# Kernel optimization log

Hardware: AMD Instinct MI355X
Metric: run time of the kernel (lower is better)

## Reference

```python
import jax, jax.numpy as jnp
import numpy as np
from jax import lax

# pywt db4 decomposition lowpass filter
_DEC_LO_NP = np.array([-0.010597401784997278, 0.032883011666982945,
                        0.030841381835986965, -0.18703481171888114,
                        -0.02798376941698385, 0.6308807679295904,
                        0.7148465705525415, 0.23037781330885523], dtype=np.float32)
_SIGNS = np.array([(-1.0) ** (k + 1) for k in range(8)], dtype=np.float32)
DEC_LO = jnp.asarray(_DEC_LO_NP)                    # dec_lo
DEC_HI = jnp.asarray(_DEC_LO_NP[::-1] * _SIGNS)     # dec_hi (QMF)
LF = 8
MAX_LEVEL = 4
# analysis kernels: torch cross-correlates with reversed dec filters == true conv
H_ANA = jnp.stack([DEC_LO[::-1], DEC_HI[::-1]])[:, None, :]  # (2,1,LF)
# synthesis: torch conv_transpose with rec filters == xcorr(dilated x, flip(rec)) = xcorr with dec
G0F = DEC_LO[None, None, :]
G1F = DEC_HI[None, None, :]
DN = ('NCH', 'OIH', 'NCH')


def _dwt_step(x):
    # x: (N, Lx) -> (lo, hi) each (N, outsize); pytorch_wavelets afb1d, mode='symmetric'
    N = x.shape[-1]
    outsize = (N + LF - 1) // 2          # pywt.dwt_coeff_len
    p = 2 * (outsize - 1) - N + LF
    xp = jnp.pad(x, ((0, 0), (p // 2, (p + 1) // 2)), mode='symmetric')
    y = lax.conv_general_dilated(xp[:, None, :], H_ANA, (2,), 'VALID',
                                 dimension_numbers=DN)  # (N,2,outsize)
    return y[:, 0, :], y[:, 1, :]


def _idwt_step(lo, hi):
    # pytorch_wavelets sfb1d: conv_transpose(stride=2, padding=LF-2)
    # == lhs-dilated xcorr with flipped rec filters (= dec filters), pad 1 each side
    y0 = lax.conv_general_dilated(lo[:, None, :], G0F, (1,), [(1, 1)],
                                  lhs_dilation=(2,), dimension_numbers=DN)
    y1 = lax.conv_general_dilated(hi[:, None, :], G1F, (1,), [(1, 1)],
                                  lhs_dilation=(2,), dimension_numbers=DN)
    return (y0 + y1)[:, 0, :]            # (N, 2*Llo + 2 - LF)


def dywpe(x, proj_w, proj_b, scale_emb, gate_w, gate_b):
    B, L, _ = x.shape
    d_model = scale_emb.shape[1]
    # channel_proj -> mono signal (B, L)
    x_mono = (jnp.einsum('blc,oc->blo', x, proj_w) + proj_b)[..., 0]
    # multi-level DWT
    lo = x_mono
    highs = []
    for _ in range(MAX_LEVEL):
        lo, hi = _dwt_step(lo)
        highs.append(hi)
    # gates: sigmoid(g) * tanh(v), per scale -> (MAX_LEVEL+1, d_model)
    gated = scale_emb @ gate_w.T + gate_b
    g, v = jnp.split(gated, 2, axis=-1)
    gates = jax.nn.sigmoid(g) * jnp.tanh(v)

    def mod(coef, gate):  # (B,Lc) x (d,) -> (B*d, Lc): outer product, fold d into batch
        return (coef[:, None, :] * gate[None, :, None]).reshape(B * d_model, -1)

    x0 = mod(lo, gates[0])
    hs = [mod(highs[i], gates[i + 1]) for i in range(MAX_LEVEL)]
    # IDWT, coarsest level first
    for h in hs[::-1]:
        if x0.shape[-1] > h.shape[-1]:
            x0 = x0[:, :h.shape[-1]]
        x0 = _idwt_step(x0, h)
    pe = x0.reshape(B, d_model, -1).transpose(0, 2, 1)  # (B, L', d_model)
    if pe.shape[1] < L:
        pe = jnp.pad(pe, ((0, 0), (0, L - pe.shape[1]), (0, 0)))
    elif pe.shape[1] > L:
        pe = pe[:, :L]
    return pe


def setup_inputs() -> dict:
    key = jax.random.key(0)
    ks = jax.random.split(key, 6)
    B, L, d_x, d_model, J = 32, 4096, 8, 512, 4
    return {
        'x': jax.random.normal(ks[0], (B, L, d_x), dtype=jnp.float32),
        'proj_w': jax.random.normal(ks[1], (1, d_x), dtype=jnp.float32) * 0.3,
        'proj_b': jax.random.normal(ks[2], (1,), dtype=jnp.float32) * 0.02,
        'scale_emb': jax.random.normal(ks[3], (J + 1, d_model), dtype=jnp.float32),
        'gate_w': jax.random.normal(ks[4], (2 * d_model, d_model), dtype=jnp.float32) * 0.04,
        'gate_b': jax.random.normal(ks[5], (2 * d_model,), dtype=jnp.float32) * 0.02,
    }


def reference(x, proj_w, proj_b, scale_emb, gate_w, gate_b):
    return dywpe(x, proj_w, proj_b, scale_emb, gate_w, gate_b)
```

## Files before the change

kernel.cpp:

```cpp
#include <hip/hip_runtime.h>

#define NB    32
#define LSEQ  4096
#define DM    512
#define ROWS  64
#define CHUNKS (LSEQ / ROWS)

typedef float f32x4 __attribute__((ext_vector_type(4)));

__device__ __constant__ float c_DL[8] = {
    -0.010597401784997278f,  0.032883011666982945f,  0.030841381835986965f,
    -0.18703481171888114f,  -0.02798376941698385f,   0.6308807679295904f,
     0.7148465705525415f,    0.23037781330885523f};
__device__ __constant__ float c_DH[8] = {
    -0.23037781330885523f,   0.7148465705525415f,   -0.6308807679295904f,
    -0.02798376941698385f,   0.18703481171888114f,   0.030841381835986965f,
    -0.032883011666982945f, -0.010597401784997278f};

__device__ __forceinline__ int imin(int a, int b) { return a < b ? a : b; }
__device__ __forceinline__ int imax(int a, int b) { return a > b ? a : b; }

__device__ __forceinline__ int reflect_idx(int i, int N) {
    if (i < 0)  i = -1 - i;
    if (i >= N) i = 2 * N - 1 - i;
    return i;
}

template <bool HI>
__device__ void fwd_range_w(const float* __restrict__ src, int src_lo, int Nsrc,
                            float* __restrict__ dst, int d_lo, int d_hi, int lane) {
    for (int t = d_lo + lane; t <= d_hi; t += 64) {
        int base = 2 * t - 6;
        float acc = 0.f;
#pragma unroll
        for (int k = 0; k < 8; ++k) {
            float xv = src[reflect_idx(base + k, Nsrc) - src_lo];
            acc = fmaf(xv, HI ? c_DH[7 - k] : c_DL[7 - k], acc);
        }
        dst[t - d_lo] = acc;
    }
}

template <bool HI>
__device__ void inv_range_w(const float* __restrict__ c, int c_lo,
                            float* __restrict__ y, int y_lo, int y_hi, int lane) {
    for (int t = y_lo + lane; t <= y_hi; t += 64) {
        int base = (t >> 1) - c_lo;
        int odd = t & 1;
        float f0 = odd ? (HI ? c_DH[0] : c_DL[0]) : (HI ? c_DH[1] : c_DL[1]);
        float f1 = odd ? (HI ? c_DH[2] : c_DL[2]) : (HI ? c_DH[3] : c_DL[3]);
        float f2 = odd ? (HI ? c_DH[4] : c_DL[4]) : (HI ? c_DH[5] : c_DL[5]);
        float f3 = odd ? (HI ? c_DH[6] : c_DL[6]) : (HI ? c_DH[7] : c_DL[7]);
        float acc = c[base] * f0;
        acc = fmaf(c[base + 1], f1, acc);
        acc = fmaf(c[base + 2], f2, acc);
        acc = fmaf(c[base + 3], f3, acc);
        y[t - y_lo] = acc;
    }
}

__global__ __launch_bounds__(1024) void gates_kernel(
    const float* __restrict__ scale_emb, const float* __restrict__ gate_w,
    const float* __restrict__ gate_b, float* __restrict__ gates) {
    int lane = threadIdx.x & 63;
    int c = blockIdx.x * 16 + (threadIdx.x >> 6);
    const float4* rg = (const float4*)(gate_w + (size_t)c * DM) + lane * 2;
    const float4* rv = (const float4*)(gate_w + (size_t)(c + DM) * DM) + lane * 2;
    float4 a0 = rg[0], a1 = rg[1];
    float4 b0 = rv[0], b1 = rv[1];
    float gacc[5], vacc[5];
#pragma unroll
    for (int j = 0; j < 5; ++j) {
        const float4* sj = (const float4*)(scale_emb + (size_t)j * DM) + lane * 2;
        float4 s0 = sj[0], s1 = sj[1];
        float ga;
        ga = s0.x * a0.x;            ga = fmaf(s0.y, a0.y, ga);
        ga = fmaf(s0.z, a0.z, ga);   ga = fmaf(s0.w, a0.w, ga);
        ga = fmaf(s1.x, a1.x, ga);   ga = fmaf(s1.y, a1.y, ga);
        ga = fmaf(s1.z, a1.z, ga);   ga = fmaf(s1.w, a1.w, ga);
        float va;
        va = s0.x * b0.x;            va = fmaf(s0.y, b0.y, va);
        va = fmaf(s0.z, b0.z, va);   va = fmaf(s0.w, b0.w, va);
        va = fmaf(s1.x, b1.x, va);   va = fmaf(s1.y, b1.y, va);
        va = fmaf(s1.z, b1.z, va);   va = fmaf(s1.w, b1.w, va);
        gacc[j] = ga;
        vacc[j] = va;
    }
#pragma unroll
    for (int j = 0; j < 5; ++j) {
#pragma unroll
        for (int off = 32; off > 0; off >>= 1) {
            gacc[j] += __shfl_xor(gacc[j], off, 64);
            vacc[j] += __shfl_xor(vacc[j], off, 64);
        }
    }
    if (lane == 0) {
        float bg = gate_b[c], bv = gate_b[DM + c];
#pragma unroll
        for (int j = 0; j < 5; ++j) {
            float g = gacc[j] + bg;
            float v = vacc[j] + bv;
            float sg = 1.f / (1.f + expf(-g));
            gates[j * DM + c] = sg * tanhf(v);
        }
    }
}

__global__ __launch_bounds__(256, 4) void fused_kernel(
    const float* __restrict__ x, const float* __restrict__ proj_w,
    const float* __restrict__ proj_b, const float* __restrict__ gates,
    float* __restrict__ out) {
    __shared__ float GL[5 * DM];
    __shared__ float XW[288];
    __shared__ float LO1[140], LO2[68], LO3[32];
    __shared__ float HI1[36], H2W[24], H3W[16], L4W[12], H4W[12];
    __shared__ float AW[16], A4W[16], A3W[24], BW[24], B4W[24];
    __shared__ float P0W[36], P2W[36], P3W[36], P4W[36];
    __shared__ float SJ[5 * ROWS];

    int bid = blockIdx.x;
    int b  = bid >> 6;
    int l0 = (bid & 63) * ROWS;

    int p0 = l0 >> 1,  p1 = ((l0 + ROWS - 1) >> 1) + 3;
    int b0 = p0 >> 1,  b1 = (p1 >> 1) + 3;
    int a0 = b0 >> 1,  a1 = (b1 >> 1) + 3;
    int w0 = a0 >> 1,  w1 = (a1 >> 1) + 3;
    int t3lo = imax(imin(imin(2 * w0 - 6, a0), 517), 0);
    int t3hi = imin(imax(imax(2 * w1 + 1, a1), 0), 517);
    int t2lo = imax(imin(2 * t3lo - 6, 2 * a0 - 6), 0);
    int t2hi = imin(imax(2 * t3hi + 1, 2 * a1 + 1), 1028);
    int t1lo = imax(imin(2 * t2lo - 6, 2 * b0 - 6), 0);
    int t1hi = imin(imax(2 * t2hi + 1, 2 * b1 + 1), 2050);
    int txlo = imax(imin(2 * t1lo - 6, 2 * p0 - 6), 0);
    int txhi = imin(imax(2 * t1hi + 1, 2 * p1 + 1), 4095);

    int wid = threadIdx.x >> 6;
    int lane = threadIdx.x & 63;

    if (wid != 0) {
        for (int i = (threadIdx.x - 64); i < 5 * DM / 4; i += 192)
            ((f32x4*)GL)[i] = ((const f32x4*)gates)[i];
    } else {
        float w[8];
#pragma unroll
        for (int k = 0; k < 8; ++k) w[k] = proj_w[k];
        float pb = proj_b[0];
        const float* xb = x + (size_t)b * LSEQ * 8;
        for (int i = txlo + lane; i <= txhi; i += 64) {
            const float4* xv = (const float4*)(xb + (size_t)i * 8);
            float4 q0 = xv[0], q1 = xv[1];
            float acc = pb;
            acc = fmaf(q0.x, w[0], acc); acc = fmaf(q0.y, w[1], acc);
            acc = fmaf(q0.z, w[2], acc); acc = fmaf(q0.w, w[3], acc);
            acc = fmaf(q1.x, w[4], acc); acc = fmaf(q1.y, w[5], acc);
            acc = fmaf(q1.z, w[6], acc); acc = fmaf(q1.w, w[7], acc);
            XW[i - txlo] = acc;
        }
        fwd_range_w<false>(XW, txlo, 4096, LO1, t1lo, t1hi, lane);
        fwd_range_w<true >(XW, txlo, 4096, HI1, p0, p1, lane);
        fwd_range_w<false>(LO1, t1lo, 2051, LO2, t2lo, t2hi, lane);
        fwd_range_w<true >(LO1, t1lo, 2051, H2W, b0, b1, lane);
        fwd_range_w<false>(LO2, t2lo, 1029, LO3, t3lo, t3hi, lane);
        fwd_range_w<true >(LO2, t2lo, 1029, H3W, a0, a1, lane);
        fwd_range_w<false>(LO3, t3lo, 518, L4W, w0, w1, lane);
        fwd_range_w<true >(LO3, t3lo, 518, H4W, w0, w1, lane);
        inv_range_w<false>(L4W, w0, AW,  a0, a1, lane);
        inv_range_w<true >(H4W, w0, A4W, a0, a1, lane);
        inv_range_w<true >(H3W, a0, A3W, b0, b1, lane);
        inv_range_w<true >(H2W, b0, P2W, p0, p1, lane);
        inv_range_w<false>(AW,  a0, BW,  b0, b1, lane);
        inv_range_w<false>(A4W, a0, B4W, b0, b1, lane);
        inv_range_w<false>(A3W, b0, P3W, p0, p1, lane);
        inv_range_w<false>(BW,  b0, P0W, p0, p1, lane);
        inv_range_w<false>(B4W, b0, P4W, p0, p1, lane);
    }
    __syncthreads();

    for (int idx = threadIdx.x; idx < 5 * ROWS; idx += 256) {
        int j = idx >> 6;
        int r = idx & (ROWS - 1);
        int l = l0 + r;
        int base = (l >> 1) - p0;
        int odd = l & 1;
        const float* Pj = (j == 0) ? P0W : (j == 1) ? HI1 :
                          (j == 2) ? P2W : (j == 3) ? P3W : P4W;
        bool hi = (j == 1);
        float f0 = odd ? (hi ? c_DH[0] : c_DL[0]) : (hi ? c_DH[1] : c_DL[1]);
        float f1 = odd ? (hi ? c_DH[2] : c_DL[2]) : (hi ? c_DH[3] : c_DL[3]);
        float f2 = odd ? (hi ? c_DH[4] : c_DL[4]) : (hi ? c_DH[5] : c_DL[5]);
        float f3 = odd ? (hi ? c_DH[6] : c_DL[6]) : (hi ? c_DH[7] : c_DL[7]);
        float acc = Pj[base] * f0;
        acc = fmaf(Pj[base + 1], f1, acc);
        acc = fmaf(Pj[base + 2], f2, acc);
        acc = fmaf(Pj[base + 3], f3, acc);
        SJ[idx] = acc;
    }
    __syncthreads();

    int half = threadIdx.x >> 7;
    int c4 = threadIdx.x & 127;
    f32x4 g0 = ((const f32x4*)(GL + 0 * DM))[c4];
    f32x4 g1 = ((const f32x4*)(GL + 1 * DM))[c4];
    f32x4 g2 = ((const f32x4*)(GL + 2 * DM))[c4];
    f32x4 g3 = ((const f32x4*)(GL + 3 * DM))[c4];
    f32x4 g4 = ((const f32x4*)(GL + 4 * DM))[c4];

    size_t rowbase = (size_t)b * LSEQ + l0;
#pragma unroll 4
    for (int r = 0; r < ROWS / 2; ++r) {
        int rr = r * 2 + half;
        float s0 = SJ[rr];
        float s1 = SJ[64 + rr];
        float s2 = SJ[128 + rr];
        float s3 = SJ[192 + rr];
        float s4 = SJ[256 + rr];
        f32x4 acc;
        acc.x = fmaf(s4, g4.x, fmaf(s3, g3.x, fmaf(s2, g2.x, fmaf(s1, g1.x, s0 * g0.x))));
        acc.y = fmaf(s4, g4.y, fmaf(s3, g3.y, fmaf(s2, g2.y, fmaf(s1, g1.y, s0 * g0.y))));
        acc.z = fmaf(s4, g4.z, fmaf(s3, g3.z, fmaf(s2, g2.z, fmaf(s1, g1.z, s0 * g0.z))));
        acc.w = fmaf(s4, g4.w, fmaf(s3, g3.w, fmaf(s2, g2.w, fmaf(s1, g1.w, s0 * g0.w))));
        __builtin_nontemporal_store(acc, (f32x4*)out + (rowbase + rr) * (DM / 4) + c4);
    }
}

extern "C" void kernel_launch(void* const* d_in, const int* in_sizes, int n_in,
                              void* d_out, int out_size, void* d_ws, size_t ws_size,
                              hipStream_t stream) {
    const float* x         = (const float*)d_in[0];
    const float* proj_w    = (const float*)d_in[1];
    const float* proj_b    = (const float*)d_in[2];
    const float* scale_emb = (const float*)d_in[3];
    const float* gate_w    = (const float*)d_in[4];
    const float* gate_b    = (const float*)d_in[5];
    float* out   = (float*)d_out;
    float* gates = (float*)d_ws;

    gates_kernel<<<32, 1024, 0, stream>>>(scale_emb, gate_w, gate_b, gates);
    fused_kernel<<<NB * CHUNKS, 256, 0, stream>>>(x, proj_w, proj_b, gates, out);
}
```

Baseline: 67.96 us.

## Split wavelet cone work across all four waves with per-wave sub-chunks

Each block now covers 128 rows instead of 64, and each of its four waves computes the wavelet dependency cone for its own 32-row slice in a private shared-memory region. Before, one wave did all of the wavelet work while the other three only loaded gates. The goal is to remove that serial single-wave stretch and halve the number of blocks, so the gates table is loaded and reused over more output rows. The cost is redundant halo computation: each 32-row cone carries almost the same filter overlap as a 64-row one.

New measurement: 66.30 us. -2.4%, faster.

```diff
diff --git a/kernel.cpp b/kernel.cpp
--- a/kernel.cpp
+++ b/kernel.cpp
@@ -3,8 +3,9 @@
 #define NB    32
 #define LSEQ  4096
 #define DM    512
-#define ROWS  64
-#define CHUNKS (LSEQ / ROWS)
+#define WROWS 32
+#define BROWS 128
+#define NBLK  (NB * LSEQ / BROWS)
 
 typedef float f32x4 __attribute__((ext_vector_type(4)));
 
@@ -16,6 +17,26 @@
     -0.23037781330885523f,   0.7148465705525415f,   -0.6308807679295904f,
     -0.02798376941698385f,   0.18703481171888114f,   0.030841381835986965f,
     -0.032883011666982945f, -0.010597401784997278f};
+
+#define O_XW   0
+#define O_LO1  240
+#define O_LO2  360
+#define O_LO3  416
+#define O_HI1  440
+#define O_H2   460
+#define O_H3   476
+#define O_L4   488
+#define O_H4   498
+#define O_A    508
+#define O_A4   520
+#define O_A3   532
+#define O_B    548
+#define O_B4   564
+#define O_P0   580
+#define O_P2   600
+#define O_P3   620
+#define O_P4   640
+#define CONE_STRIDE 672
 
 __device__ __forceinline__ int imin(int a, int b) { return a < b ? a : b; }
 __device__ __forceinline__ int imax(int a, int b) { return a > b ? a : b; }
@@ -111,21 +132,23 @@
     const float* __restrict__ proj_b, const float* __restrict__ gates,
     float* __restrict__ out) {
     __shared__ float GL[5 * DM];
-    __shared__ float XW[288];
-    __shared__ float LO1[140], LO2[68], LO3[32];
-    __shared__ float HI1[36], H2W[24], H3W[16], L4W[12], H4W[12];
-    __shared__ float AW[16], A4W[16], A3W[24], BW[24], B4W[24];
-    __shared__ float P0W[36], P2W[36], P3W[36], P4W[36];
-    __shared__ float SJ[5 * ROWS];
+    __shared__ float CB[4][CONE_STRIDE];
+    __shared__ float SJ[5 * BROWS];
 
     int bid = blockIdx.x;
-    int b  = bid >> 6;
-    int l0 = (bid & 63) * ROWS;
-
-    int p0 = l0 >> 1,  p1 = ((l0 + ROWS - 1) >> 1) + 3;
-    int b0 = p0 >> 1,  b1 = (p1 >> 1) + 3;
-    int a0 = b0 >> 1,  a1 = (b1 >> 1) + 3;
-    int w0 = a0 >> 1,  w1 = (a1 >> 1) + 3;
+    int b  = bid >> 5;
+    int l0 = (bid & 31) * BROWS;
+    int wid = threadIdx.x >> 6;
+    int lane = threadIdx.x & 63;
+    int l0w = l0 + wid * WROWS;
+
+    for (int i = threadIdx.x; i < 5 * DM / 4; i += 256)
+        ((f32x4*)GL)[i] = ((const f32x4*)gates)[i];
+
+    int p0 = l0w >> 1,  p1 = ((l0w + WROWS - 1) >> 1) + 3;
+    int b0 = p0 >> 1,   b1 = (p1 >> 1) + 3;
+    int a0 = b0 >> 1,   a1 = (b1 >> 1) + 3;
+    int w0 = a0 >> 1,   w1 = (a1 >> 1) + 3;
     int t3lo = imax(imin(imin(2 * w0 - 6, a0), 517), 0);
     int t3hi = imin(imax(imax(2 * w1 + 1, a1), 0), 517);
     int t2lo = imax(imin(2 * t3lo - 6, 2 * a0 - 6), 0);
@@ -135,13 +158,9 @@
     int txlo = imax(imin(2 * t1lo - 6, 2 * p0 - 6), 0);
     int txhi = imin(imax(2 * t1hi + 1, 2 * p1 + 1), 4095);
 
-    int wid = threadIdx.x >> 6;
-    int lane = threadIdx.x & 63;
-
-    if (wid != 0) {
-        for (int i = (threadIdx.x - 64); i < 5 * DM / 4; i += 192)
-            ((f32x4*)GL)[i] = ((const f32x4*)gates)[i];
-    } else {
+    float* W = CB[wid];
+
+    {
         float w[8];
 #pragma unroll
         for (int k = 0; k < 8; ++k) w[k] = proj_w[k];
@@ -155,36 +174,37 @@
             acc = fmaf(q0.z, w[2], acc); acc = fmaf(q0.w, w[3], acc);
             acc = fmaf(q1.x, w[4], acc); acc = fmaf(q1.y, w[5], acc);
             acc = fmaf(q1.z, w[6], acc); acc = fmaf(q1.w, w[7], acc);
-            XW[i - txlo] = acc;
-        }
-        fwd_range_w<false>(XW, txlo, 4096, LO1, t1lo, t1hi, lane);
-        fwd_range_w<true >(XW, txlo, 4096, HI1, p0, p1, lane);
-        fwd_range_w<false>(LO1, t1lo, 2051, LO2, t2lo, t2hi, lane);
-        fwd_range_w<true >(LO1, t1lo, 2051, H2W, b0, b1, lane);
-        fwd_range_w<false>(LO2, t2lo, 1029, LO3, t3lo, t3hi, lane);
-        fwd_range_w<true >(LO2, t2lo, 1029, H3W, a0, a1, lane);
-        fwd_range_w<false>(LO3, t3lo, 518, L4W, w0, w1, lane);
-        fwd_range_w<true >(LO3, t3lo, 518, H4W, w0, w1, lane);
-        inv_range_w<false>(L4W, w0, AW,  a0, a1, lane);
-        inv_range_w<true >(H4W, w0, A4W, a0, a1, lane);
-        inv_range_w<true >(H3W, a0, A3W, b0, b1, lane);
-        inv_range_w<true >(H2W, b0, P2W, p0, p1, lane);
-        inv_range_w<false>(AW,  a0, BW,  b0, b1, lane);
-        inv_range_w<false>(A4W, a0, B4W, b0, b1, lane);
-        inv_range_w<false>(A3W, b0, P3W, p0, p1, lane);
-        inv_range_w<false>(BW,  b0, P0W, p0, p1, lane);
-        inv_range_w<false>(B4W, b0, P4W, p0, p1, lane);
-    }
-    __syncthreads();
-
-    for (int idx = threadIdx.x; idx < 5 * ROWS; idx += 256) {
-        int j = idx >> 6;
-        int r = idx & (ROWS - 1);
-        int l = l0 + r;
+            W[O_XW + i - txlo] = acc;
+        }
+    }
+
+    fwd_range_w<false>(W + O_XW, txlo, 4096, W + O_LO1, t1lo, t1hi, lane);
+    fwd_range_w<true >(W + O_XW, txlo, 4096, W + O_HI1, p0, p1, lane);
+    fwd_range_w<false>(W + O_LO1, t1lo, 2051, W + O_LO2, t2lo, t2hi, lane);
+    fwd_range_w<true >(W + O_LO1, t1lo, 2051, W + O_H2, b0, b1, lane);
+    fwd_range_w<false>(W + O_LO2, t2lo, 1029, W + O_LO3, t3lo, t3hi, lane);
+    fwd_range_w<true >(W + O_LO2, t2lo, 1029, W + O_H3, a0, a1, lane);
+    fwd_range_w<false>(W + O_LO3, t3lo, 518, W + O_L4, w0, w1, lane);
+    fwd_range_w<true >(W + O_LO3, t3lo, 518, W + O_H4, w0, w1, lane);
+
+    inv_range_w<false>(W + O_L4, w0, W + O_A,  a0, a1, lane);
+    inv_range_w<true >(W + O_H4, w0, W + O_A4, a0, a1, lane);
+    inv_range_w<true >(W + O_H3, a0, W + O_A3, b0, b1, lane);
+    inv_range_w<true >(W + O_H2, b0, W + O_P2, p0, p1, lane);
+    inv_range_w<false>(W + O_A,  a0, W + O_B,  b0, b1, lane);
+    inv_range_w<false>(W + O_A4, a0, W + O_B4, b0, b1, lane);
+    inv_range_w<false>(W + O_A3, b0, W + O_P3, p0, p1, lane);
+    inv_range_w<false>(W + O_B,  b0, W + O_P0, p0, p1, lane);
+    inv_range_w<false>(W + O_B4, b0, W + O_P4, p0, p1, lane);
+
+    for (int idx = lane; idx < 5 * WROWS; idx += 64) {
+        int j = idx >> 5;
+        int r = idx & (WROWS - 1);
+        int l = l0w + r;
         int base = (l >> 1) - p0;
         int odd = l & 1;
-        const float* Pj = (j == 0) ? P0W : (j == 1) ? HI1 :
-                          (j == 2) ? P2W : (j == 3) ? P3W : P4W;
+        const float* Pj = (j == 0) ? (W + O_P0) : (j == 1) ? (W + O_HI1) :
+                          (j == 2) ? (W + O_P2) : (j == 3) ? (W + O_P3) : (W + O_P4);
         bool hi = (j == 1);
         float f0 = odd ? (hi ? c_DH[0] : c_DL[0]) : (hi ? c_DH[1] : c_DL[1]);
         float f1 = odd ? (hi ? c_DH[2] : c_DL[2]) : (hi ? c_DH[3] : c_DL[3]);
@@ -194,7 +214,7 @@
         acc = fmaf(Pj[base + 1], f1, acc);
         acc = fmaf(Pj[base + 2], f2, acc);
         acc = fmaf(Pj[base + 3], f3, acc);
-        SJ[idx] = acc;
+        SJ[j * BROWS + wid * WROWS + r] = acc;
     }
     __syncthreads();
 
@@ -208,13 +228,13 @@
 
     size_t rowbase = (size_t)b * LSEQ + l0;
 #pragma unroll 4
-    for (int r = 0; r < ROWS / 2; ++r) {
+    for (int r = 0; r < BROWS / 2; ++r) {
         int rr = r * 2 + half;
         float s0 = SJ[rr];
-        float s1 = SJ[64 + rr];
-        float s2 = SJ[128 + rr];
-        float s3 = SJ[192 + rr];
-        float s4 = SJ[256 + rr];
+        float s1 = SJ[BROWS + rr];
+        float s2 = SJ[2 * BROWS + rr];
+        float s3 = SJ[3 * BROWS + rr];
+        float s4 = SJ[4 * BROWS + rr];
         f32x4 acc;
         acc.x = fmaf(s4, g4.x, fmaf(s3, g3.x, fmaf(s2, g2.x, fmaf(s1, g1.x, s0 * g0.x))));
         acc.y = fmaf(s4, g4.y, fmaf(s3, g3.y, fmaf(s2, g2.y, fmaf(s1, g1.y, s0 * g0.y))));
@@ -237,5 +257,5 @@
     float* gates = (float*)d_ws;
 
     gates_kernel<<<32, 1024, 0, stream>>>(scale_emb, gate_w, gate_b, gates);
-    fused_kernel<<<NB * CHUNKS, 256, 0, stream>>>(x, proj_w, proj_b, gates, out);
-}
+    fused_kernel<<<NBLK, 256, 0, stream>>>(x, proj_w, proj_b, gates, out);
+}
```
